# Performance work log

Measured on AMD Instinct MI355X. Metric: run time of the kernel, lower is better.

## Reference

```python
import jax, jax.numpy as jnp
import numpy as np

B, S, HID, NH, HD, E, K = 8, 1024, 1024, 16, 64, 8, 2
IDIM = 2 * HD  # expert internal dim
EPS = 1e-5


def layer_norm(x, g, b):
    m = jnp.mean(x, axis=-1, keepdims=True)
    v = jnp.mean(jnp.square(x - m), axis=-1, keepdims=True)
    return (x - m) * jax.lax.rsqrt(v + EPS) * g + b


def setup_inputs() -> dict:
    key = jax.random.key(0)
    ks = jax.random.split(key, 12)
    n = jax.random.normal
    return {
        "queries": n(ks[0], (B, S, HID), jnp.float32),
        "keys": n(ks[1], (B, S, HID), jnp.float32),
        "values": n(ks[2], (B, S, HID), jnp.float32),
        "memorys": n(ks[3], (B, NH, S, HD), jnp.float32),
        "Wq": n(ks[4], (HD, HD), jnp.float32) * 0.02,
        "Wk": n(ks[5], (HD, HD), jnp.float32) * 0.02,
        "Wv": n(ks[6], (HD, HD), jnp.float32) * 0.02,
        "forget_gate": n(ks[7], (HD,), jnp.float32),
        "gate_W": n(ks[8], (E, HD), jnp.float32) * 0.02,
        "gate_b": jnp.zeros((E,), jnp.float32),
        "ln1_g": jnp.ones((E, HD), jnp.float32),
        "ln1_b": jnp.zeros((E, HD), jnp.float32),
        "W1": n(ks[9], (E, IDIM, HD), jnp.float32) * 0.02,
        "ln2_g": jnp.ones((E, IDIM), jnp.float32),
        "ln2_b": jnp.zeros((E, IDIM), jnp.float32),
        "W2": n(ks[10], (E, HD, IDIM), jnp.float32) * 0.02,
        "b2": jnp.zeros((E, HD), jnp.float32),
    }


def reference(queries, keys, values, memorys, Wq, Wk, Wv, forget_gate,
              gate_W, gate_b, ln1_g, ln1_b, W1, ln2_g, ln2_b, W2, b2):
    bsz, seq, _ = queries.shape
    gelu = lambda x: jax.nn.gelu(x, approximate=False)

    # head split: [B,S,HID] -> [B,NH,S,HD]
    q = queries.reshape(bsz, seq, NH, HD).transpose(0, 2, 1, 3)
    k = keys.reshape(bsz, seq, NH, HD).transpose(0, 2, 1, 3)
    v = values.reshape(bsz, seq, NH, HD).transpose(0, 2, 1, 3)

    q_ = q @ Wq.T
    k_ = k @ Wk.T
    v_ = v @ Wv.T

    # gated memory cell
    cell = k_ * v_ + forget_gate * memorys
    current_memorys = (1.0 - forget_gate) * cell + forget_gate * memorys
    cell_values = q_ * current_memorys  # [B,NH,S,HD]

    # token-mixing MoE (per-token, over last dim)
    x = cell_values.reshape(-1, HD)  # [N, HD], N = B*NH*S
    logits = x @ gate_W.T + gate_b  # [N, E]
    topv, topi = jax.lax.top_k(logits, K)  # [N, K]
    # sparse combine weights [N, E] (raw gate values, as in the original)
    w = jnp.sum(jax.nn.one_hot(topi, E, dtype=x.dtype) * topv[..., None], axis=1)

    def expert_fwd(g1, b1, w1, g2, b2_, w2, bias2):
        h = gelu(layer_norm(x, g1, b1)) @ w1.T      # [N, IDIM]
        h = gelu(layer_norm(h, g2, b2_)) @ w2.T + bias2  # [N, HD]
        return h

    all_out = jax.vmap(expert_fwd)(ln1_g, ln1_b, W1, ln2_g, ln2_b, W2, b2)  # [E,N,HD]
    moe = jnp.einsum('ne,end->nd', w, all_out)  # [N, HD]

    token_mixing = moe.reshape(bsz, NH, seq, HD).transpose(0, 2, 1, 3).reshape(bsz, seq, NH * HD)
    return token_mixing, current_memorys
```

## Files before the change

### kernel.cpp

```cpp
#include <hip/hip_runtime.h>
#include <stdint.h>

typedef unsigned short u16;
typedef unsigned int   u32;
typedef unsigned long long u64;
typedef __attribute__((ext_vector_type(8))) short short8;
typedef __attribute__((ext_vector_type(4))) short s16x4;
typedef __attribute__((ext_vector_type(4))) float f32x4;

#define B_    8
#define S_    1024
#define HID_  1024
#define NH_   16
#define HD_   64
#define E_    8
#define IDIM_ 128
#define NTOK  (B_*NH_*S_)

#define CSTRIDE 16

__device__ __forceinline__ float bf2f(u16 u){ return __uint_as_float(((u32)u) << 16); }
__device__ __forceinline__ u16 f2bf(float f){
    u32 u = __float_as_uint(f);
    u32 r = u + 0x7fffu + ((u >> 16) & 1u);
    return (u16)(r >> 16);
}
__device__ __forceinline__ short8 frag8(const float* __restrict__ p){
    float4 a = *(const float4*)p;
    float4 b = *(const float4*)(p + 4);
    short8 r;
    r[0]=(short)f2bf(a.x); r[1]=(short)f2bf(a.y); r[2]=(short)f2bf(a.z); r[3]=(short)f2bf(a.w);
    r[4]=(short)f2bf(b.x); r[5]=(short)f2bf(b.y); r[6]=(short)f2bf(b.z); r[7]=(short)f2bf(b.w);
    return r;
}
__device__ __forceinline__ float gelu_exact(float x){
    return 0.5f * x * (1.0f + erff(x * 0.70710678118654752f));
}
__device__ __forceinline__ float gelu_f(float x){
    float z = 1.5957691216057308f * (x + 0.044715f * x * x * x);
    float e = __expf(z);
    float t = 1.0f - 2.0f / (e + 1.0f);
    return 0.5f * x * (1.0f + t);
}

__global__ void k_zero(u32* c){
    c[threadIdx.x] = 0;
}

__global__ __launch_bounds__(256) void k_prep(
    const float* __restrict__ W1, const float* __restrict__ W2,
    u16* __restrict__ wB1, u16* __restrict__ wB2)
{
    const int i = blockIdx.x*256 + threadIdx.x;
    wB1[i] = f2bf(W1[i]);
    wB2[i] = f2bf(W2[i]);
}

__global__ __launch_bounds__(256,2) void k_mem(
    const float* __restrict__ kin, const float* __restrict__ vin, const float* __restrict__ mem,
    const float* __restrict__ Wk,  const float* __restrict__ Wv,  const float* __restrict__ fg,
    float* __restrict__ cur_out)
{
    const int lane = threadIdx.x & 63;
    const int wid  = threadIdx.x >> 6;
    const int m    = lane & 15;
    const int kg   = lane >> 4;

    const int slab  = blockIdx.x;
    const int chunk = slab & 3, h = (slab >> 2) & 15, b = slab >> 6;
    const int tw    = chunk*256 + wid*64;

    const float* kbase = kin + ((size_t)b*S_)*HID_ + h*64;
    const float* vbase = vin + ((size_t)b*S_)*HID_ + h*64;

    f32x4 accK[4][4], accV[4][4];
    const f32x4 z = {0.f,0.f,0.f,0.f};
    #pragma unroll
    for (int i=0;i<4;i++){ accK[i][0]=z;accK[i][1]=z;accK[i][2]=z;accK[i][3]=z;
                           accV[i][0]=z;accV[i][1]=z;accV[i][2]=z;accV[i][3]=z; }

    #pragma unroll
    for (int kk=0; kk<2; kk++){
        const int k0 = kk*32 + kg*8;
        short8 aF[4], bF[4];
        #pragma unroll
        for (int mt=0; mt<4; mt++) aF[mt] = frag8(kbase + (size_t)(tw + mt*16 + m)*HID_ + k0);
        #pragma unroll
        for (int ct=0; ct<4; ct++) bF[ct] = frag8(Wk + (ct*16 + m)*64 + k0);
        #pragma unroll
        for (int mt=0; mt<4; mt++)
            #pragma unroll
            for (int ct=0; ct<4; ct++)
                accK[mt][ct] = __builtin_amdgcn_mfma_f32_16x16x32_bf16(aF[mt], bF[ct], accK[mt][ct], 0,0,0);
    }
    #pragma unroll
    for (int kk=0; kk<2; kk++){
        const int k0 = kk*32 + kg*8;
        short8 aF[4], bF[4];
        #pragma unroll
        for (int mt=0; mt<4; mt++) aF[mt] = frag8(vbase + (size_t)(tw + mt*16 + m)*HID_ + k0);
        #pragma unroll
        for (int ct=0; ct<4; ct++) bF[ct] = frag8(Wv + (ct*16 + m)*64 + k0);
        #pragma unroll
        for (int mt=0; mt<4; mt++)
            #pragma unroll
            for (int ct=0; ct<4; ct++)
                accV[mt][ct] = __builtin_amdgcn_mfma_f32_16x16x32_bf16(aF[mt], bF[ct], accV[mt][ct], 0,0,0);
    }

    const size_t nb = ((size_t)(b*NH_ + h)) << 10;
    float fgv[4];
    #pragma unroll
    for (int ct=0; ct<4; ct++) fgv[ct] = fg[ct*16 + m];

    #pragma unroll
    for (int mt=0; mt<4; mt++){
        #pragma unroll
        for (int r=0; r<4; r++){
            const int tok = tw + mt*16 + kg*4 + r;
            const size_t rowo = (nb + (size_t)tok)*64;
            #pragma unroll
            for (int ct=0; ct<4; ct++){
                const int d = ct*16 + m;
                const float kd = accK[mt][ct][r];
                const float vd = accV[mt][ct][r];
                const float f  = fgv[ct];
                const float mv = mem[rowo + d];
                const float cell = kd*vd + f*mv;
                cur_out[rowo + d] = (1.0f - f)*cell + f*mv;
            }
        }
    }
}

__global__ __launch_bounds__(256,2) void k_q(
    const float* __restrict__ qin, const float* __restrict__ cur_in, const float* __restrict__ Wq,
    float* __restrict__ out0)
{
    const int lane = threadIdx.x & 63;
    const int wid  = threadIdx.x >> 6;
    const int m    = lane & 15;
    const int kg   = lane >> 4;

    const int slab  = blockIdx.x;
    const int chunk = slab & 3, h = (slab >> 2) & 15, b = slab >> 6;
    const int tw    = chunk*256 + wid*64;

    const float* qbase = qin + ((size_t)b*S_)*HID_ + h*64;

    f32x4 accQ[4][4];
    const f32x4 z = {0.f,0.f,0.f,0.f};
    #pragma unroll
    for (int i=0;i<4;i++){ accQ[i][0]=z;accQ[i][1]=z;accQ[i][2]=z;accQ[i][3]=z; }

    #pragma unroll
    for (int kk=0; kk<2; kk++){
        const int k0 = kk*32 + kg*8;
        short8 aF[4], bF[4];
        #pragma unroll
        for (int mt=0; mt<4; mt++) aF[mt] = frag8(qbase + (size_t)(tw + mt*16 + m)*HID_ + k0);
        #pragma unroll
        for (int ct=0; ct<4; ct++) bF[ct] = frag8(Wq + (ct*16 + m)*64 + k0);
        #pragma unroll
        for (int mt=0; mt<4; mt++)
            #pragma unroll
            for (int ct=0; ct<4; ct++)
                accQ[mt][ct] = __builtin_amdgcn_mfma_f32_16x16x32_bf16(aF[mt], bF[ct], accQ[mt][ct], 0,0,0);
    }

    const size_t nb = ((size_t)(b*NH_ + h)) << 10;
    #pragma unroll
    for (int mt=0; mt<4; mt++){
        #pragma unroll
        for (int r=0; r<4; r++){
            const int tok = tw + mt*16 + kg*4 + r;
            const size_t curo = (nb + (size_t)tok)*64;
            const size_t po   = ((size_t)(b*S_ + tok)*NH_ + h)*64;
            #pragma unroll
            for (int ct=0; ct<4; ct++){
                const int d = ct*16 + m;
                out0[po + d] = accQ[mt][ct][r] * cur_in[curo + d];
            }
        }
    }
}

__global__ __launch_bounds__(256,2) void k_gate(
    const float* __restrict__ x_src, const float* __restrict__ gW, const float* __restrict__ gB,
    uint4* __restrict__ topiv, u32* __restrict__ counts)
{
    __shared__ float sGW[512], sGB[8];
    __shared__ u32 sWc[4][8];
    const int tid = threadIdx.x;
    for (int i = tid; i < 512; i += 256) sGW[i] = gW[i];
    if (tid < 8) sGB[tid] = gB[tid];
    __syncthreads();

    const int n = blockIdx.x*256 + tid;
    const int s = n & (S_-1), h = (n >> 10) & (NH_-1), b = n >> 14;
    const size_t po = ((size_t)(b*S_ + s)*NH_ + h)*64;

    float lg[8];
    #pragma unroll
    for (int e = 0; e < 8; e++) lg[e] = sGB[e];

    for (int dc = 0; dc < 16; dc++){
        float4 x4 = ((const float4*)(x_src + po))[dc];
        float xv[4] = {x4.x, x4.y, x4.z, x4.w};
        #pragma unroll
        for (int i = 0; i < 4; i++){
            const int d = dc*4 + i;
            #pragma unroll
            for (int e = 0; e < 8; e++) lg[e] += sGW[e*64 + d] * xv[i];
        }
    }

    int i1 = 0; float v1 = lg[0];
    #pragma unroll
    for (int e = 1; e < 8; e++){ if (lg[e] > v1){ v1 = lg[e]; i1 = e; } }
    int i2 = -1; float v2 = -3.0e38f;
    #pragma unroll
    for (int e = 0; e < 8; e++){ if (e != i1 && lg[e] > v2){ v2 = lg[e]; i2 = e; } }

    topiv[n] = make_uint4((u32)i1, (u32)i2, __float_as_uint(v1), __float_as_uint(v2));

    const int lane = tid & 63;
    const int w    = tid >> 6;
    #pragma unroll
    for (int e = 0; e < 8; e++){
        u64 m1 = __ballot(i1 == e);
        u64 m2 = __ballot(i2 == e);
        if (lane == 0) sWc[w][e] = (u32)(__popcll(m1) + __popcll(m2));
    }
    __syncthreads();
    if (tid < 8){
        u32 t = sWc[0][tid] + sWc[1][tid] + sWc[2][tid] + sWc[3][tid];
        if (t) atomicAdd(&counts[tid*CSTRIDE], t);
    }
}

__global__ __launch_bounds__(256,2) void k_scatter(
    const uint4* __restrict__ topiv, const u32* __restrict__ counts, u32* __restrict__ cursors,
    u32* __restrict__ bucket, int2* __restrict__ slots)
{
    __shared__ u32 sC1[4][8], sC2[4][8];
    __shared__ u32 sB1[4][8], sB2[4][8];

    const int tid = threadIdx.x;
    const int n = blockIdx.x*256 + tid;
    uint4 t = topiv[n];
    const int i1 = (int)t.x, i2 = (int)t.y;

    int off[8]; int acc = 0;
    #pragma unroll
    for (int e = 0; e < 8; e++){ off[e] = acc; acc += (int)counts[e*CSTRIDE]; }

    const int s = n & (S_-1), h = (n >> 10) & (NH_-1), b = n >> 14;
    const u32 pos32 = (u32)((b*S_ + s)*NH_ + h);

    const int lane = tid & 63;
    const int w    = tid >> 6;
    const u64 low = (1ull << lane) - 1ull;

    u64 myM1 = 0, myM2 = 0;
    #pragma unroll
    for (int e = 0; e < 8; e++){
        u64 m1 = __ballot(i1 == e);
        u64 m2 = __ballot(i2 == e);
        if (i1 == e) myM1 = m1;
        if (i2 == e) myM2 = m2;
        if (lane == 0){ sC1[w][e] = (u32)__popcll(m1); sC2[w][e] = (u32)__popcll(m2); }
    }
    __syncthreads();

    if (tid < 8){
        const int e = tid;
        u32 tot = 0;
        #pragma unroll
        for (int ww = 0; ww < 4; ww++) tot += sC1[ww][e] + sC2[ww][e];
        u32 base = tot ? atomicAdd(&cursors[e*CSTRIDE], tot) : 0;
        u32 run = base;
        #pragma unroll
        for (int ww = 0; ww < 4; ww++){
            sB1[ww][e] = run; run += sC1[ww][e];
            sB2[ww][e] = run; run += sC2[ww][e];
        }
    }
    __syncthreads();

    const int slot1 = off[i1] + (int)sB1[w][i1] + (int)__popcll(myM1 & low);
    const int slot2 = off[i2] + (int)sB2[w][i2] + (int)__popcll(myM2 & low);

    bucket[slot1] = pos32;
    bucket[slot2] = pos32;
    slots[n] = make_int2(slot1, slot2);
}

__global__ __launch_bounds__(256,3) void k_expert_mfma(
    const float* __restrict__ x_src, const u32* __restrict__ bucket, const u32* __restrict__ counts,
    const u16* __restrict__ wB1, const u16* __restrict__ wB2,
    const float* __restrict__ l1g, const float* __restrict__ l1b,
    const float* __restrict__ l2g, const float* __restrict__ l2b,
    const float* __restrict__ b2,  u16* __restrict__ aout)
{
    const int e = blockIdx.x >> 10;
    const int c = blockIdx.x & 1023;
    const int cnt = (int)counts[e*CSTRIDE];
    const int aBase = c * 128;
    if (aBase >= cnt) return;

    int off = 0;
    #pragma unroll
    for (int ee = 0; ee < 8; ee++){ if (ee < e) off += (int)counts[ee*CSTRIDE]; }

    __shared__ __align__(16) u16 sA1[128*64];
    __shared__ __align__(16) u16 sH [128*128];
    __shared__ float2 sStat[2*128];
    __shared__ u32   sPos[128];
    __shared__ float sL1g[64], sL1b[64], sL2g[128], sL2b[128], sB2[64];

    const int tid = threadIdx.x;
    if (tid < 64){ sL1g[tid] = l1g[e*64+tid]; sL1b[tid] = l1b[e*64+tid]; sB2[tid] = b2[e*64+tid]; }
    else if (tid < 192){ int t = tid - 64; sL2g[t] = l2g[e*128+t]; sL2b[t] = l2b[e*128+t]; }
    if (tid < 128){
        int a = aBase + tid; if (a > cnt-1) a = cnt-1;
        sPos[tid] = bucket[off + a];
    }
    __syncthreads();

    {
        const int q = tid & 15;
        #pragma unroll
        for (int it = 0; it < 8; it++){
            const int tok = it*16 + (tid >> 4);
            const u32 pos = sPos[tok];
            float4 x4 = *(const float4*)(x_src + ((size_t)pos << 6) + q*4);
            float s0 = x4.x + x4.y + x4.z + x4.w;
            float s1 = x4.x*x4.x + x4.y*x4.y + x4.z*x4.z + x4.w*x4.w;
            #pragma unroll
            for (int msk = 1; msk < 16; msk <<= 1){
                s0 += __shfl_xor(s0, msk);
                s1 += __shfl_xor(s1, msk);
            }
            const float mu = s0 * (1.0f/64.0f);
            const float rs = rsqrtf(s1 * (1.0f/64.0f) - mu*mu + 1e-5f);
            s16x4 pk;
            pk[0] = (short)f2bf(gelu_f((x4.x - mu)*rs*sL1g[q*4+0] + sL1b[q*4+0]));
            pk[1] = (short)f2bf(gelu_f((x4.y - mu)*rs*sL1g[q*4+1] + sL1b[q*4+1]));
            pk[2] = (short)f2bf(gelu_f((x4.z - mu)*rs*sL1g[q*4+2] + sL1b[q*4+2]));
            pk[3] = (short)f2bf(gelu_f((x4.w - mu)*rs*sL1g[q*4+3] + sL1b[q*4+3]));
            *(s16x4*)((char*)sA1 + (((tok<<7) + (q<<3)) ^ ((tok&7)<<4))) = pk;
        }
    }
    __syncthreads();

    const int lane = tid & 63;
    const int w    = tid >> 6;
    const int m    = lane & 15;
    const int kg   = lane >> 4;
    const int th   = w >> 1;
    const int nh   = w & 1;

    f32x4 acc[4][4];
    const f32x4 z = {0.f,0.f,0.f,0.f};
    #pragma unroll
    for (int i=0;i<4;i++){ acc[i][0]=z;acc[i][1]=z;acc[i][2]=z;acc[i][3]=z; }

    const u16* wB1e = wB1 + e*8192;
    #pragma unroll
    for (int kk = 0; kk < 2; kk++){
        const int k0 = kk*32 + kg*8;
        short8 aF[4], bF[4];
        #pragma unroll
        for (int mt = 0; mt < 4; mt++){
            const int row = th*64 + mt*16 + m;
            aF[mt] = *(const short8*)((const char*)sA1 + (((row<<7) + (k0<<1)) ^ ((row&7)<<4)));
        }
        #pragma unroll
        for (int ct = 0; ct < 4; ct++)
            bF[ct] = *(const short8*)(wB1e + (nh*64 + ct*16 + m)*64 + k0);
        #pragma unroll
        for (int mt = 0; mt < 4; mt++)
            #pragma unroll
            for (int ct = 0; ct < 4; ct++)
                acc[mt][ct] = __builtin_amdgcn_mfma_f32_16x16x32_bf16(aF[mt], bF[ct], acc[mt][ct], 0,0,0);
    }

    #pragma unroll
    for (int mt = 0; mt < 4; mt++){
        #pragma unroll
        for (int r = 0; r < 4; r++){
            float v0 = acc[mt][0][r], v1 = acc[mt][1][r], v2 = acc[mt][2][r], v3 = acc[mt][3][r];
            float p0 = (v0+v1)+(v2+v3);
            float p1 = (v0*v0+v1*v1)+(v2*v2+v3*v3);
            #pragma unroll
            for (int msk = 1; msk < 16; msk <<= 1){
                p0 += __shfl_xor(p0, msk);
                p1 += __shfl_xor(p1, msk);
            }
            if (m == 0){
                const int row = th*64 + mt*16 + kg*4 + r;
                sStat[nh*128 + row] = make_float2(p0, p1);
            }
        }
    }
    __syncthreads();

    #pragma unroll
    for (int mt = 0; mt < 4; mt++){
        #pragma unroll
        for (int r = 0; r < 4; r++){
            const int row = th*64 + mt*16 + kg*4 + r;
            const float2 a0 = sStat[row];
            const float2 a1 = sStat[128 + row];
            const float s0 = a0.x + a1.x, s1 = a0.y + a1.y;
            const float mu = s0 * (1.0f/128.0f);
            const float rs = rsqrtf(s1 * (1.0f/128.0f) - mu*mu + 1e-5f);
            #pragma unroll
            for (int ct = 0; ct < 4; ct++){
                const int col = nh*64 + ct*16 + m;
                *(u16*)((char*)sH + (((row<<8) + (col<<1)) ^ ((row&7)<<4)))
                    = f2bf(gelu_f((acc[mt][ct][r] - mu)*rs*sL2g[col] + sL2b[col]));
            }
        }
    }
    __syncthreads();

    f32x4 acc2[2][4];
    #pragma unroll
    for (int i=0;i<2;i++){ acc2[i][0]=z;acc2[i][1]=z;acc2[i][2]=z;acc2[i][3]=z; }

    const u16* wB2e = wB2 + e*8192;
    #pragma unroll
    for (int kk = 0; kk < 4; kk++){
        const int k0 = kk*32 + kg*8;
        short8 aF[2], bF[4];
        #pragma unroll
        for (int mt = 0; mt < 2; mt++){
            const int row = w*32 + mt*16 + m;
            aF[mt] = *(const short8*)((const char*)sH + (((row<<8) + (k0<<1)) ^ ((row&7)<<4)));
        }
        #pragma unroll
        for (int ct = 0; ct < 4; ct++)
            bF[ct] = *(const short8*)(wB2e + (ct*16 + m)*128 + k0);
        #pragma unroll
        for (int mt = 0; mt < 2; mt++)
            #pragma unroll
            for (int ct = 0; ct < 4; ct++)
                acc2[mt][ct] = __builtin_amdgcn_mfma_f32_16x16x32_bf16(aF[mt], bF[ct], acc2[mt][ct], 0,0,0);
    }

    #pragma unroll
    for (int mt = 0; mt < 2; mt++){
        #pragma unroll
        for (int r = 0; r < 4; r++){
            const int row = w*32 + mt*16 + kg*4 + r;
            #pragma unroll
            for (int ct = 0; ct < 4; ct++){
                const int col = ct*16 + m;
                *(u16*)((char*)sA1 + (((row<<7) + (col<<1)) ^ ((row&7)<<4)))
                    = f2bf(acc2[mt][ct][r] + sB2[col]);
            }
        }
    }
    __syncthreads();

    #pragma unroll
    for (int it = 0; it < 4; it++){
        const int idx = it*256 + tid;
        const int row = idx >> 3, qq = idx & 7;
        if (aBase + row < cnt){
            uint4 v = *(const uint4*)((const char*)sA1 + (((row<<7) + (qq<<4)) ^ ((row&7)<<4)));
            *(uint4*)(aout + ((size_t)(off + aBase + row) << 6) + qq*8) = v;
        }
    }
}

__global__ __launch_bounds__(256,2) void k_expert(
    const float* __restrict__ x_src, const u32* __restrict__ bucket, const u32* __restrict__ counts,
    const float* __restrict__ W1,  const float* __restrict__ W2,
    const float* __restrict__ l1g, const float* __restrict__ l1b,
    const float* __restrict__ l2g, const float* __restrict__ l2b,
    const float* __restrict__ b2,  u16* __restrict__ aout)
{
    const int e = blockIdx.x >> 9;
    const int c = blockIdx.x & 511;
    const int cnt = (int)counts[e*CSTRIDE];
    const int aBase = c * 256;
    if (aBase >= cnt) return;

    int off = 0;
    for (int ee = 0; ee < 8; ee++){ if (ee < e) off += (int)counts[ee*CSTRIDE]; }

    __shared__ float sW1[8192];
    __shared__ float sW2T[128*68];
    __shared__ float sL1g[64], sL1b[64], sL2g[128], sL2b[128], sB2[64];
    const int tid = threadIdx.x;
    for (int i = tid; i < 8192; i += 256){
        sW1[i] = W1[e*8192 + i];
        int d = i >> 7, j = i & 127;
        sW2T[j*68 + d] = W2[e*8192 + i];
    }
    if (tid < 64){ sL1g[tid] = l1g[e*64+tid]; sL1b[tid] = l1b[e*64+tid]; sB2[tid] = b2[e*64+tid]; }
    if (tid < 128){ sL2g[tid] = l2g[e*128+tid]; sL2b[tid] = l2b[e*128+tid]; }
    __syncthreads();

    const int a = aBase + tid;
    if (a >= cnt) return;
    const u32 pos32 = bucket[off + a];

    float g[64];
    #pragma unroll
    for (int i = 0; i < 16; i++){
        float4 t = ((const float4*)(x_src + (size_t)pos32*64))[i];
        g[i*4+0]=t.x; g[i*4+1]=t.y; g[i*4+2]=t.z; g[i*4+3]=t.w;
    }

    float s0 = 0.f, s1 = 0.f;
    #pragma unroll
    for (int d = 0; d < 64; d++){ s0 += g[d]; s1 += g[d]*g[d]; }
    float m  = s0 * (1.0f/64.0f);
    float va = s1 * (1.0f/64.0f) - m*m;
    float rs = rsqrtf(va + 1e-5f);
    #pragma unroll
    for (int d = 0; d < 64; d++) g[d] = gelu_exact((g[d]-m)*rs*sL1g[d] + sL1b[d]);

    u32 hpk[64];
    float hs = 0.f, hs2 = 0.f;
    for (int jp = 0; jp < 64; jp++){
        float h0, h1;
        {
            float a0=0.f,a1=0.f,a2=0.f,a3=0.f;
            const float4* w4 = (const float4*)&sW1[(2*jp)*64];
            #pragma unroll
            for (int i = 0; i < 16; i++){
                float4 ww = w4[i];
                a0 += ww.x*g[i*4+0]; a1 += ww.y*g[i*4+1]; a2 += ww.z*g[i*4+2]; a3 += ww.w*g[i*4+3];
            }
            h0 = (a0+a1)+(a2+a3);
        }
        {
            float a0=0.f,a1=0.f,a2=0.f,a3=0.f;
            const float4* w4 = (const float4*)&sW1[(2*jp+1)*64];
            #pragma unroll
            for (int i = 0; i < 16; i++){
                float4 ww = w4[i];
                a0 += ww.x*g[i*4+0]; a1 += ww.y*g[i*4+1]; a2 += ww.z*g[i*4+2]; a3 += ww.w*g[i*4+3];
            }
            h1 = (a0+a1)+(a2+a3);
        }
        hs += h0 + h1; hs2 += h0*h0 + h1*h1;
        hpk[jp] = (u32)f2bf(h0) | ((u32)f2bf(h1) << 16);
    }
    float m2  = hs  * (1.0f/128.0f);
    float va2 = hs2 * (1.0f/128.0f) - m2*m2;
    float rs2 = rsqrtf(va2 + 1e-5f);

    float acc[64];
    #pragma unroll
    for (int d = 0; d < 64; d++) acc[d] = sB2[d];
    for (int j = 0; j < 128; j++){
        float hj = bf2f((u16)((j & 1) ? (hpk[j>>1] >> 16) : (hpk[j>>1] & 0xffffu)));
        float gh = gelu_exact((hj - m2)*rs2*sL2g[j] + sL2b[j]);
        const float4* w2t = (const float4*)&sW2T[j*68];
        #pragma unroll
        for (int d4 = 0; d4 < 16; d4++){
            float4 w = w2t[d4];
            acc[d4*4+0] += gh * w.x;
            acc[d4*4+1] += gh * w.y;
            acc[d4*4+2] += gh * w.z;
            acc[d4*4+3] += gh * w.w;
        }
    }

    u16* op = aout + (size_t)(off + a) * 64;
    #pragma unroll
    for (int dc = 0; dc < 8; dc++){
        uint4 o;
        o.x = (u32)f2bf(acc[dc*8+0]) | ((u32)f2bf(acc[dc*8+1]) << 16);
        o.y = (u32)f2bf(acc[dc*8+2]) | ((u32)f2bf(acc[dc*8+3]) << 16);
        o.z = (u32)f2bf(acc[dc*8+4]) | ((u32)f2bf(acc[dc*8+5]) << 16);
        o.w = (u32)f2bf(acc[dc*8+6]) | ((u32)f2bf(acc[dc*8+7]) << 16);
        ((uint4*)op)[dc] = o;
    }
}

__global__ __launch_bounds__(256,4) void k_combine(
    const u16* __restrict__ aout, const uint4* __restrict__ topiv,
    const int2* __restrict__ slots, float* __restrict__ out0)
{
    const int tid = threadIdx.x;
    const int p   = blockIdx.x*16 + (tid >> 4);
    const int cq  = tid & 15;

    const int h  = p & (NH_-1);
    const int bs = p >> 4;
    const int b  = bs >> 10, s = bs & (S_-1);
    const int n  = ((b*NH_ + h) << 10) + s;

    uint4 t = topiv[n];
    float w1 = __uint_as_float(t.z), w2 = __uint_as_float(t.w);
    int2 sl = slots[n];

    uint2 ua = *(const uint2*)(aout + (size_t)sl.x*64 + cq*4);
    uint2 ub = *(const uint2*)(aout + (size_t)sl.y*64 + cq*4);

    float4 o;
    o.x = w1*bf2f((u16)(ua.x & 0xffffu)) + w2*bf2f((u16)(ub.x & 0xffffu));
    o.y = w1*bf2f((u16)(ua.x >> 16))     + w2*bf2f((u16)(ub.x >> 16));
    o.z = w1*bf2f((u16)(ua.y & 0xffffu)) + w2*bf2f((u16)(ub.y & 0xffffu));
    o.w = w1*bf2f((u16)(ua.y >> 16))     + w2*bf2f((u16)(ub.y >> 16));
    *(float4*)(out0 + (size_t)p*64 + cq*4) = o;
}

extern "C" void kernel_launch(void* const* d_in, const int* in_sizes, int n_in,
                              void* d_out, int out_size, void* d_ws, size_t ws_size,
                              hipStream_t stream)
{
    const float* qin = (const float*)d_in[0];
    const float* kin = (const float*)d_in[1];
    const float* vin = (const float*)d_in[2];
    const float* mem = (const float*)d_in[3];
    const float* Wq  = (const float*)d_in[4];
    const float* Wk  = (const float*)d_in[5];
    const float* Wv  = (const float*)d_in[6];
    const float* fg  = (const float*)d_in[7];
    const float* gW  = (const float*)d_in[8];
    const float* gB  = (const float*)d_in[9];
    const float* l1g = (const float*)d_in[10];
    const float* l1b = (const float*)d_in[11];
    const float* W1  = (const float*)d_in[12];
    const float* l2g = (const float*)d_in[13];
    const float* l2b = (const float*)d_in[14];
    const float* W2  = (const float*)d_in[15];
    const float* b2  = (const float*)d_in[16];

    float* out0 = (float*)d_out;
    float* out1 = out0 + (size_t)NTOK * 64;

    char* ws = (char*)d_ws;
    u16*   aout   = (u16*)(ws);
    uint4* topiv  = (uint4*)(ws + (size_t)33554432);
    int2*  slots  = (int2*)(ws + (size_t)35651584);
    u32*   bucket = (u32*)(ws + (size_t)36700160);
    u32*   counts = (u32*)(ws + (size_t)37748736);
    u32*   cursors = (u32*)(ws + (size_t)37749248);
    u16*   wB1    = (u16*)(ws + (size_t)37749760);
    u16*   wB2    = (u16*)(ws + (size_t)37880832);
    const size_t WS_NEED = 38011904;

    (void)in_sizes; (void)n_in; (void)out_size;

    const bool use_mfma = (ws_size >= WS_NEED);

    k_zero   <<<1, 256, 0, stream>>>(counts);
    if (use_mfma)
        k_prep <<<256, 256, 0, stream>>>(W1, W2, wB1, wB2);
    k_mem    <<<512, 256, 0, stream>>>(kin, vin, mem, Wk, Wv, fg, out1);
    k_q      <<<512, 256, 0, stream>>>(qin, out1, Wq, out0);
    k_gate   <<<NTOK/256, 256, 0, stream>>>(out0, gW, gB, topiv, counts);
    k_scatter<<<NTOK/256, 256, 0, stream>>>(topiv, counts, cursors, bucket, slots);
    if (use_mfma)
        k_expert_mfma<<<E_*1024, 256, 0, stream>>>(out0, bucket, counts, wB1, wB2,
                                                   l1g, l1b, l2g, l2b, b2, aout);
    else
        k_expert <<<E_*512, 256, 0, stream>>>(out0, bucket, counts, W1, W2,
                                              l1g, l1b, l2g, l2b, b2, aout);
    k_combine<<<NTOK/16, 256, 0, stream>>>(aout, topiv, slots, out0);
}
```

Measured before the change: 339.7 us.

## Make expert MFMA kernel wave-private to drop block barriers and LDS staging

Each wave now owns 32 tokens end to end. It loads the gathered x rows straight into MFMA A-fragments in registers, applying LayerNorm and GELU there, instead of staging them through shared memory. It computes all 128 hidden columns itself, so the second LayerNorm's statistics need no cross-wave shared reduction. This removes most __syncthreads and the sA1/sStat buffers and shrinks LDS to per-wave tiles, in exchange for more accumulator registers (16 f32x4) and per-wave redundant weight loads.

```diff
diff --git a/kernel.cpp b/kernel.cpp
--- a/kernel.cpp
+++ b/kernel.cpp
@@ -244,7 +244,7 @@
     u32* __restrict__ bucket, int2* __restrict__ slots)
 {
     __shared__ u32 sC1[4][8], sC2[4][8];
-    __shared__ u32 sB1[4][8], sB2[4][8];
+    __shared__ u32 sB1[4][8], sB2w[4][8];
 
     const int tid = threadIdx.x;
     const int n = blockIdx.x*256 + tid;
@@ -283,13 +283,13 @@
         #pragma unroll
         for (int ww = 0; ww < 4; ww++){
             sB1[ww][e] = run; run += sC1[ww][e];
-            sB2[ww][e] = run; run += sC2[ww][e];
+            sB2w[ww][e] = run; run += sC2[ww][e];
         }
     }
     __syncthreads();
 
     const int slot1 = off[i1] + (int)sB1[w][i1] + (int)__popcll(myM1 & low);
-    const int slot2 = off[i2] + (int)sB2[w][i2] + (int)__popcll(myM2 & low);
+    const int slot2 = off[i2] + (int)sB2w[w][i2] + (int)__popcll(myM2 & low);
 
     bucket[slot1] = pos32;
     bucket[slot2] = pos32;
@@ -313,165 +313,153 @@
     #pragma unroll
     for (int ee = 0; ee < 8; ee++){ if (ee < e) off += (int)counts[ee*CSTRIDE]; }
 
-    __shared__ __align__(16) u16 sA1[128*64];
-    __shared__ __align__(16) u16 sH [128*128];
-    __shared__ float2 sStat[2*128];
-    __shared__ u32   sPos[128];
+    __shared__ __align__(16) u16 sH[4][32*128];
     __shared__ float sL1g[64], sL1b[64], sL2g[128], sL2b[128], sB2[64];
 
     const int tid = threadIdx.x;
     if (tid < 64){ sL1g[tid] = l1g[e*64+tid]; sL1b[tid] = l1b[e*64+tid]; sB2[tid] = b2[e*64+tid]; }
     else if (tid < 192){ int t = tid - 64; sL2g[t] = l2g[e*128+t]; sL2b[t] = l2b[e*128+t]; }
-    if (tid < 128){
-        int a = aBase + tid; if (a > cnt-1) a = cnt-1;
-        sPos[tid] = bucket[off + a];
-    }
-    __syncthreads();
-
-    {
-        const int q = tid & 15;
-        #pragma unroll
-        for (int it = 0; it < 8; it++){
-            const int tok = it*16 + (tid >> 4);
-            const u32 pos = sPos[tok];
-            float4 x4 = *(const float4*)(x_src + ((size_t)pos << 6) + q*4);
-            float s0 = x4.x + x4.y + x4.z + x4.w;
-            float s1 = x4.x*x4.x + x4.y*x4.y + x4.z*x4.z + x4.w*x4.w;
-            #pragma unroll
-            for (int msk = 1; msk < 16; msk <<= 1){
-                s0 += __shfl_xor(s0, msk);
-                s1 += __shfl_xor(s1, msk);
-            }
-            const float mu = s0 * (1.0f/64.0f);
-            const float rs = rsqrtf(s1 * (1.0f/64.0f) - mu*mu + 1e-5f);
-            s16x4 pk;
-            pk[0] = (short)f2bf(gelu_f((x4.x - mu)*rs*sL1g[q*4+0] + sL1b[q*4+0]));
-            pk[1] = (short)f2bf(gelu_f((x4.y - mu)*rs*sL1g[q*4+1] + sL1b[q*4+1]));
-            pk[2] = (short)f2bf(gelu_f((x4.z - mu)*rs*sL1g[q*4+2] + sL1b[q*4+2]));
-            pk[3] = (short)f2bf(gelu_f((x4.w - mu)*rs*sL1g[q*4+3] + sL1b[q*4+3]));
-            *(s16x4*)((char*)sA1 + (((tok<<7) + (q<<3)) ^ ((tok&7)<<4))) = pk;
-        }
-    }
     __syncthreads();
 
     const int lane = tid & 63;
     const int w    = tid >> 6;
     const int m    = lane & 15;
     const int kg   = lane >> 4;
-    const int th   = w >> 1;
-    const int nh   = w & 1;
-
-    f32x4 acc[4][4];
+    const int tb   = aBase + w*32;
+    char* sHw = (char*)(&sH[w][0]);
+
+    int pos[2];
+    #pragma unroll
+    for (int t = 0; t < 2; t++){
+        int a = tb + t*16 + m; if (a > cnt-1) a = cnt-1;
+        pos[t] = (int)bucket[off + a];
+    }
+
+    short8 aF[2][2];
+    #pragma unroll
+    for (int t = 0; t < 2; t++){
+        const float* rp = x_src + ((size_t)(u32)pos[t] << 6);
+        float4 v0 = *(const float4*)(rp + kg*8);
+        float4 v1 = *(const float4*)(rp + kg*8 + 4);
+        float4 v2 = *(const float4*)(rp + 32 + kg*8);
+        float4 v3 = *(const float4*)(rp + 32 + kg*8 + 4);
+        float s0 = (v0.x+v0.y+v0.z+v0.w) + (v1.x+v1.y+v1.z+v1.w)
+                 + (v2.x+v2.y+v2.z+v2.w) + (v3.x+v3.y+v3.z+v3.w);
+        float s1 = (v0.x*v0.x+v0.y*v0.y+v0.z*v0.z+v0.w*v0.w)
+                 + (v1.x*v1.x+v1.y*v1.y+v1.z*v1.z+v1.w*v1.w)
+                 + (v2.x*v2.x+v2.y*v2.y+v2.z*v2.z+v2.w*v2.w)
+                 + (v3.x*v3.x+v3.y*v3.y+v3.z*v3.z+v3.w*v3.w);
+        s0 += __shfl_xor(s0, 16); s0 += __shfl_xor(s0, 32);
+        s1 += __shfl_xor(s1, 16); s1 += __shfl_xor(s1, 32);
+        const float mu = s0 * (1.0f/64.0f);
+        const float rs = rsqrtf(s1 * (1.0f/64.0f) - mu*mu + 1e-5f);
+        float xv[16] = {v0.x,v0.y,v0.z,v0.w, v1.x,v1.y,v1.z,v1.w,
+                        v2.x,v2.y,v2.z,v2.w, v3.x,v3.y,v3.z,v3.w};
+        #pragma unroll
+        for (int kk = 0; kk < 2; kk++){
+            short8 f;
+            #pragma unroll
+            for (int j = 0; j < 8; j++){
+                const int k = kk*32 + kg*8 + j;
+                f[j] = (short)f2bf(gelu_f((xv[kk*8+j] - mu)*rs*sL1g[k] + sL1b[k]));
+            }
+            aF[t][kk] = f;
+        }
+    }
+
     const f32x4 z = {0.f,0.f,0.f,0.f};
-    #pragma unroll
-    for (int i=0;i<4;i++){ acc[i][0]=z;acc[i][1]=z;acc[i][2]=z;acc[i][3]=z; }
+    f32x4 acc1[2][8];
+    #pragma unroll
+    for (int t = 0; t < 2; t++)
+        #pragma unroll
+        for (int ct = 0; ct < 8; ct++) acc1[t][ct] = z;
 
     const u16* wB1e = wB1 + e*8192;
     #pragma unroll
     for (int kk = 0; kk < 2; kk++){
         const int k0 = kk*32 + kg*8;
-        short8 aF[4], bF[4];
-        #pragma unroll
-        for (int mt = 0; mt < 4; mt++){
-            const int row = th*64 + mt*16 + m;
-            aF[mt] = *(const short8*)((const char*)sA1 + (((row<<7) + (k0<<1)) ^ ((row&7)<<4)));
-        }
-        #pragma unroll
-        for (int ct = 0; ct < 4; ct++)
-            bF[ct] = *(const short8*)(wB1e + (nh*64 + ct*16 + m)*64 + k0);
-        #pragma unroll
-        for (int mt = 0; mt < 4; mt++)
-            #pragma unroll
-            for (int ct = 0; ct < 4; ct++)
-                acc[mt][ct] = __builtin_amdgcn_mfma_f32_16x16x32_bf16(aF[mt], bF[ct], acc[mt][ct], 0,0,0);
-    }
-
-    #pragma unroll
-    for (int mt = 0; mt < 4; mt++){
+        short8 bF[8];
+        #pragma unroll
+        for (int ct = 0; ct < 8; ct++)
+            bF[ct] = *(const short8*)(wB1e + (ct*16 + m)*64 + k0);
+        #pragma unroll
+        for (int t = 0; t < 2; t++)
+            #pragma unroll
+            for (int ct = 0; ct < 8; ct++)
+                acc1[t][ct] = __builtin_amdgcn_mfma_f32_16x16x32_bf16(aF[t][kk], bF[ct], acc1[t][ct], 0,0,0);
+    }
+
+    #pragma unroll
+    for (int t = 0; t < 2; t++){
         #pragma unroll
         for (int r = 0; r < 4; r++){
-            float v0 = acc[mt][0][r], v1 = acc[mt][1][r], v2 = acc[mt][2][r], v3 = acc[mt][3][r];
-            float p0 = (v0+v1)+(v2+v3);
-            float p1 = (v0*v0+v1*v1)+(v2*v2+v3*v3);
+            float p0 = 0.f, p1 = 0.f;
+            #pragma unroll
+            for (int ct = 0; ct < 8; ct++){ float v = acc1[t][ct][r]; p0 += v; p1 += v*v; }
             #pragma unroll
             for (int msk = 1; msk < 16; msk <<= 1){
                 p0 += __shfl_xor(p0, msk);
                 p1 += __shfl_xor(p1, msk);
             }
-            if (m == 0){
-                const int row = th*64 + mt*16 + kg*4 + r;
-                sStat[nh*128 + row] = make_float2(p0, p1);
-            }
-        }
-    }
-    __syncthreads();
-
-    #pragma unroll
-    for (int mt = 0; mt < 4; mt++){
-        #pragma unroll
-        for (int r = 0; r < 4; r++){
-            const int row = th*64 + mt*16 + kg*4 + r;
-            const float2 a0 = sStat[row];
-            const float2 a1 = sStat[128 + row];
-            const float s0 = a0.x + a1.x, s1 = a0.y + a1.y;
-            const float mu = s0 * (1.0f/128.0f);
-            const float rs = rsqrtf(s1 * (1.0f/128.0f) - mu*mu + 1e-5f);
-            #pragma unroll
-            for (int ct = 0; ct < 4; ct++){
-                const int col = nh*64 + ct*16 + m;
-                *(u16*)((char*)sH + (((row<<8) + (col<<1)) ^ ((row&7)<<4)))
-                    = f2bf(gelu_f((acc[mt][ct][r] - mu)*rs*sL2g[col] + sL2b[col]));
-            }
-        }
-    }
-    __syncthreads();
+            const float mu = p0 * (1.0f/128.0f);
+            const float rs = rsqrtf(p1 * (1.0f/128.0f) - mu*mu + 1e-5f);
+            const int row = t*16 + kg*4 + r;
+            #pragma unroll
+            for (int ct = 0; ct < 8; ct++){
+                const int col = ct*16 + m;
+                *(u16*)(sHw + (((row<<8) + (col<<1)) ^ ((row&7)<<4)))
+                    = f2bf(gelu_f((acc1[t][ct][r] - mu)*rs*sL2g[col] + sL2b[col]));
+            }
+        }
+    }
 
     f32x4 acc2[2][4];
     #pragma unroll
-    for (int i=0;i<2;i++){ acc2[i][0]=z;acc2[i][1]=z;acc2[i][2]=z;acc2[i][3]=z; }
+    for (int t = 0; t < 2; t++)
+        #pragma unroll
+        for (int ct = 0; ct < 4; ct++) acc2[t][ct] = z;
 
     const u16* wB2e = wB2 + e*8192;
     #pragma unroll
     for (int kk = 0; kk < 4; kk++){
         const int k0 = kk*32 + kg*8;
-        short8 aF[2], bF[4];
-        #pragma unroll
-        for (int mt = 0; mt < 2; mt++){
-            const int row = w*32 + mt*16 + m;
-            aF[mt] = *(const short8*)((const char*)sH + (((row<<8) + (k0<<1)) ^ ((row&7)<<4)));
+        short8 aF2[2], bF2[4];
+        #pragma unroll
+        for (int t = 0; t < 2; t++){
+            const int row = t*16 + m;
+            aF2[t] = *(const short8*)(sHw + (((row<<8) + (k0<<1)) ^ ((row&7)<<4)));
         }
         #pragma unroll
         for (int ct = 0; ct < 4; ct++)
-            bF[ct] = *(const short8*)(wB2e + (ct*16 + m)*128 + k0);
-        #pragma unroll
-        for (int mt = 0; mt < 2; mt++)
+            bF2[ct] = *(const short8*)(wB2e + (ct*16 + m)*128 + k0);
+        #pragma unroll
+        for (int t = 0; t < 2; t++)
             #pragma unroll
             for (int ct = 0; ct < 4; ct++)
-                acc2[mt][ct] = __builtin_amdgcn_mfma_f32_16x16x32_bf16(aF[mt], bF[ct], acc2[mt][ct], 0,0,0);
-    }
-
-    #pragma unroll
-    for (int mt = 0; mt < 2; mt++){
+                acc2[t][ct] = __builtin_amdgcn_mfma_f32_16x16x32_bf16(aF2[t], bF2[ct], acc2[t][ct], 0,0,0);
+    }
+
+    #pragma unroll
+    for (int t = 0; t < 2; t++){
         #pragma unroll
         for (int r = 0; r < 4; r++){
-            const int row = w*32 + mt*16 + kg*4 + r;
+            const int row = t*16 + kg*4 + r;
             #pragma unroll
             for (int ct = 0; ct < 4; ct++){
                 const int col = ct*16 + m;
-                *(u16*)((char*)sA1 + (((row<<7) + (col<<1)) ^ ((row&7)<<4)))
-                    = f2bf(acc2[mt][ct][r] + sB2[col]);
-            }
-        }
-    }
-    __syncthreads();
+                *(u16*)(sHw + (((row<<7) + (col<<1)) ^ ((row&7)<<4)))
+                    = f2bf(acc2[t][ct][r] + sB2[col]);
+            }
+        }
+    }
 
     #pragma unroll
     for (int it = 0; it < 4; it++){
-        const int idx = it*256 + tid;
+        const int idx = it*64 + lane;
         const int row = idx >> 3, qq = idx & 7;
-        if (aBase + row < cnt){
-            uint4 v = *(const uint4*)((const char*)sA1 + (((row<<7) + (qq<<4)) ^ ((row&7)<<4)));
-            *(uint4*)(aout + ((size_t)(off + aBase + row) << 6) + qq*8) = v;
+        if (tb + row < cnt){
+            uint4 v = *(const uint4*)(sHw + (((row<<7) + (qq<<4)) ^ ((row&7)<<4)));
+            *(uint4*)(aout + ((size_t)(off + tb + row) << 6) + qq*8) = v;
         }
     }
 }
```

Result: faster. 326.9 us (-3.8%).
